# Kernel tuning notes

Measured on AMD Instinct MI355X. Metric: run time of the kernel, lower is better.

Reference implementation:

```python
import jax, jax.numpy as jnp
import numpy as np

B, N, D, H, E = 4, 1024, 1024, 2048, 8

def setup_inputs() -> dict:
    key = jax.random.key(0)
    ks = jax.random.split(key, 5)
    return {
        "x": jax.random.normal(ks[0], (B, N, D), dtype=jnp.float32),
        "gate_w": jax.random.normal(ks[1], (D, E), dtype=jnp.float32) * 0.02,
        "gate_b": jnp.zeros((E,), dtype=jnp.float32),
        "w1": jax.random.normal(ks[2], (E, D, H), dtype=jnp.float32) * 0.02,
        "b1": jnp.zeros((E, H), dtype=jnp.float32),
        "w2": jax.random.normal(ks[3], (E, H, D), dtype=jnp.float32) * 0.02,
        "b2": jnp.zeros((E, D), dtype=jnp.float32),
        "gamma": jnp.ones((D,), dtype=jnp.float32),
    }

def reference(x, gate_w, gate_b, w1, b1, w2, b2, gamma):
    b, n, d = x.shape
    e = w1.shape[0]
    xf = x.reshape(b * n, d)                                    # [T, D]
    # gate: softmax over experts, then top-1
    probs = jax.nn.softmax(xf @ gate_w + gate_b, axis=-1)       # [T, E]
    top_val = jnp.max(probs, axis=-1, keepdims=True)            # [T, 1]
    top_idx = jnp.argmax(probs, axis=-1)                        # [T]
    # all-expert FFN (dense reference for masked dispatch; dropout in eval)
    h = jax.nn.gelu(jnp.einsum('td,edh->eth', xf, w1) + b1[:, None, :],
                    approximate=False)                          # [E, T, H]
    eo = jnp.einsum('eth,ehd->etd', h, w2) + b2[:, None, :]     # [E, T, D]
    onehot = jax.nn.one_hot(top_idx, e, dtype=xf.dtype)         # [T, E]
    out = jnp.einsum('etd,te->td', eo, onehot)                  # select routed expert
    y = (xf + out * top_val).reshape(b, n, d)
    # RMSNorm: F.normalize (L2, eps=1e-12) * gamma * sqrt(dim)
    nrm = jnp.linalg.norm(y, axis=-1, keepdims=True)
    y = y / jnp.maximum(nrm, 1e-12) * gamma * np.float32(np.sqrt(d))
    # load-balancing loss (unbiased variance like torch.var)
    importance = probs.sum(axis=0)                              # [E]
    load_loss = jnp.var(importance, ddof=1) / (jnp.mean(importance) ** 2 + 1e-10)
    return jax.nn.gelu(y, approximate=False), load_loss
```

## Files before the change

kernel.cpp:

```cpp
#include <hip/hip_runtime.h>
#include <math.h>

#define T_TOK 4096
#define DIM   1024
#define HID   2048
#define NE    8
#define TMM   128
#define BK    64
#define GATE_BLOCKS (T_TOK / 4)

typedef unsigned int  u32;
typedef unsigned short u16;
typedef __attribute__((ext_vector_type(8))) short bf16x8;
typedef __attribute__((ext_vector_type(4))) float f32x4;

__device__ __forceinline__ float gelu_exact(float v) {
    return 0.5f * v * (1.0f + erff(v * 0.70710678118654752440f));
}

__device__ __forceinline__ float gelu_fast(float x) {
    float u = 1.5957691216057308f * (x + 0.044715f * x * x * x);
    float e = __expf(u);
    float t = 1.f - 2.f / (e + 1.f);
    return 0.5f * x * (1.f + t);
}

__device__ __forceinline__ u16 f2bf(float v) {
    u32 u = __float_as_uint(v);
    u32 r = (u + 0x7FFFu + ((u >> 16) & 1u)) >> 16;
    return (u16)r;
}

__device__ __forceinline__ void gld_lds16(const void* g, void* l) {
    __builtin_amdgcn_global_load_lds(
        (const __attribute__((address_space(1))) u32*)g,
        (__attribute__((address_space(3))) u32*)l,
        16, 0, 0);
}

__device__ __forceinline__ void transpose_body(
    const float* __restrict__ in, u16* __restrict__ out, int R, int C,
    int bx, int by, int bz, float (*tile)[65])
{
    const float* src = in  + (size_t)bz * R * C;
    u16*         dst = out + (size_t)bz * R * C;
    const int c0 = bx * 64, r0 = by * 64;
    const int th = threadIdx.x;

    const int tr  = th >> 4;
    const int tc4 = (th & 15) * 4;
    #pragma unroll
    for (int i = 0; i < 4; i++) {
        const int r = tr + i * 16;
        float4 v = *(const float4*)&src[(size_t)(r0 + r) * C + c0 + tc4];
        tile[r][tc4 + 0] = v.x; tile[r][tc4 + 1] = v.y;
        tile[r][tc4 + 2] = v.z; tile[r][tc4 + 3] = v.w;
    }
    __syncthreads();
    const int cc  = th >> 4;
    const int rr4 = (th & 15) * 4;
    #pragma unroll
    for (int i = 0; i < 4; i++) {
        const int c = cc + i * 16;
        ushort4 o;
        o.x = f2bf(tile[rr4 + 0][c]);
        o.y = f2bf(tile[rr4 + 1][c]);
        o.z = f2bf(tile[rr4 + 2][c]);
        o.w = f2bf(tile[rr4 + 3][c]);
        *(ushort4*)&dst[(size_t)(c0 + c) * R + r0 + rr4] = o;
    }
}

__global__ __launch_bounds__(256) void prep_kernel(
    const float* __restrict__ w1, const float* __restrict__ w2,
    u16* __restrict__ w1t, u16* __restrict__ w2t,
    const float* __restrict__ x, const float* __restrict__ gw,
    const float* __restrict__ gb, float* __restrict__ top_val,
    int* __restrict__ top_idx, float* __restrict__ partial_imp,
    int* __restrict__ partial_cnt)
{
    __shared__ float tile[64][65];
    __shared__ float s_imp[NE];
    __shared__ int   s_cnt[NE];

    const int id = blockIdx.x;
    if (id < 4096) {
        transpose_body(w1, w1t, DIM, HID, id & 31, (id >> 5) & 15, id >> 9, tile);
        return;
    }
    if (id < 8192) {
        const int i2 = id - 4096;
        transpose_body(w2, w2t, HID, DIM, i2 & 15, (i2 >> 4) & 31, i2 >> 9, tile);
        return;
    }

    const int g = id - 8192;
    if (threadIdx.x < NE) { s_imp[threadIdx.x] = 0.f; s_cnt[threadIdx.x] = 0; }
    __syncthreads();

    const int wave = threadIdx.x >> 6;
    const int lane = threadIdx.x & 63;
    const int t = g * 4 + wave;

    float acc[NE];
    #pragma unroll
    for (int e = 0; e < NE; e++) acc[e] = 0.f;

    const float* xr = x + (size_t)t * DIM;
    #pragma unroll 4
    for (int k = lane; k < DIM; k += 64) {
        float xv = xr[k];
        const float* gp = gw + (size_t)k * NE;
        float4 g0 = *(const float4*)gp;
        float4 g1 = *(const float4*)(gp + 4);
        acc[0] += xv * g0.x; acc[1] += xv * g0.y;
        acc[2] += xv * g0.z; acc[3] += xv * g0.w;
        acc[4] += xv * g1.x; acc[5] += xv * g1.y;
        acc[6] += xv * g1.z; acc[7] += xv * g1.w;
    }
    #pragma unroll
    for (int e = 0; e < NE; e++) {
        #pragma unroll
        for (int off = 32; off > 0; off >>= 1)
            acc[e] += __shfl_down(acc[e], off, 64);
    }
    if (lane == 0) {
        float l[NE];
        float m = -1e30f;
        #pragma unroll
        for (int e = 0; e < NE; e++) { l[e] = acc[e] + gb[e]; m = fmaxf(m, l[e]); }
        float s = 0.f;
        #pragma unroll
        for (int e = 0; e < NE; e++) { l[e] = expf(l[e] - m); s += l[e]; }
        float inv = 1.f / s;
        int bi = 0; float bv = -1.f;
        #pragma unroll
        for (int e = 0; e < NE; e++) {
            float p = l[e] * inv;
            atomicAdd(&s_imp[e], p);
            if (p > bv) { bv = p; bi = e; }
        }
        top_val[t] = bv;
        top_idx[t] = bi;
        atomicAdd(&s_cnt[bi], 1);
    }
    __syncthreads();
    if (threadIdx.x < NE) {
        partial_imp[g * NE + threadIdx.x] = s_imp[threadIdx.x];
        partial_cnt[g * NE + threadIdx.x] = s_cnt[threadIdx.x];
    }
}

__global__ __launch_bounds__(256) void plan_kernel(
    const float* __restrict__ partial_imp, const int* __restrict__ partial_cnt,
    int* __restrict__ counts, int* __restrict__ offsets,
    int* __restrict__ tile_e, int* __restrict__ tile_s,
    int* __restrict__ tile_rows, int* __restrict__ ntiles,
    float* __restrict__ loss_out)
{
    __shared__ float rimp[32][NE];
    __shared__ int   rcnt[32][NE];
    const int th = threadIdx.x;
    const int e = th & 7, chunk = th >> 3;
    float si = 0.f; int sc = 0;
    #pragma unroll 8
    for (int i = 0; i < GATE_BLOCKS / 32; i++) {
        const int b = chunk * (GATE_BLOCKS / 32) + i;
        si += partial_imp[b * NE + e];
        sc += partial_cnt[b * NE + e];
    }
    rimp[chunk][e] = si;
    rcnt[chunk][e] = sc;
    __syncthreads();
    if (th < NE) {
        float s = 0.f; int c = 0;
        for (int i = 0; i < 32; i++) { s += rimp[i][th]; c += rcnt[i][th]; }
        counts[th] = c;
        rimp[0][th] = s;
        rcnt[0][th] = c;
    }
    __syncthreads();
    if (th == 0) {
        int off = 0, nt = 0;
        for (int ee = 0; ee < NE; ee++) {
            offsets[ee] = off;
            const int c = rcnt[0][ee];
            for (int s = 0; s < c; s += TMM) {
                tile_e[nt] = ee;
                tile_s[nt] = off + s;
                tile_rows[nt] = min(TMM, c - s);
                nt++;
            }
            off += c;
        }
        offsets[NE] = off;
        *ntiles = nt;

        float mean = 0.f;
        for (int ee = 0; ee < NE; ee++) mean += rimp[0][ee];
        mean *= (1.0f / NE);
        float var = 0.f;
        for (int ee = 0; ee < NE; ee++) { float d = rimp[0][ee] - mean; var += d * d; }
        var *= (1.0f / (NE - 1));
        loss_out[0] = var / (mean * mean + 1e-10f);
    }
}

__global__ __launch_bounds__(256) void scatter_kernel(
    const int* __restrict__ top_idx, const int* __restrict__ offsets,
    int* __restrict__ cursors, int* __restrict__ sorted_tok)
{
    __shared__ int lcnt[NE], lbase[NE];
    if (threadIdx.x < NE) lcnt[threadIdx.x] = 0;
    __syncthreads();
    const int t = blockIdx.x * blockDim.x + threadIdx.x;
    const int e = top_idx[t];
    const int lrank = atomicAdd(&lcnt[e], 1);
    __syncthreads();
    if (threadIdx.x < NE)
        lbase[threadIdx.x] = atomicAdd(&cursors[threadIdx.x], lcnt[threadIdx.x]);
    __syncthreads();
    sorted_tok[offsets[e] + lbase[e] + lrank] = t;
}

__global__ __launch_bounds__(256) void gather_x_kernel(
    const float* __restrict__ x, const int* __restrict__ sorted_tok,
    u16* __restrict__ xs)
{
    const int s = blockIdx.x;
    const int tok = sorted_tok[s];
    const float* src = x + (size_t)tok * DIM;
    u16* dst = xs + (size_t)s * DIM;
    const int i = threadIdx.x * 4;
    float4 v = *(const float4*)&src[i];
    ushort4 o;
    o.x = f2bf(v.x); o.y = f2bf(v.y); o.z = f2bf(v.z); o.w = f2bf(v.w);
    *(ushort4*)&dst[i] = o;
}

__global__ __launch_bounds__(512, 4) void ffn1_mfma(
    const u16* __restrict__ xs, const u16* __restrict__ w1t,
    const float* __restrict__ b1,
    const int* __restrict__ tile_e, const int* __restrict__ tile_s,
    const int* __restrict__ tile_rows, const int* __restrict__ ntiles,
    u16* __restrict__ h_buf)
{
    const int tile = blockIdx.y;
    if (tile >= *ntiles) return;
    const int e     = tile_e[tile];
    const int sbase = tile_s[tile];
    const int rows  = tile_rows[tile];
    const int nbase = blockIdx.x * 256;

    __shared__ __align__(16) u16 As[128 * BK];
    __shared__ __align__(16) u16 Bs[256 * BK];

    const int th = threadIdx.x;
    const int w  = th >> 6;
    const int l  = th & 63;
    const int wm = w >> 2, wn = w & 3;
    const int lr = l >> 3;
    const int lcs = ((l & 7) ^ lr) * 8;

    const u16* aptr[2];
    #pragma unroll
    for (int c = 0; c < 2; c++) {
        int srow = sbase + c * 64 + w * 8 + lr;
        if (srow > T_TOK - 1) srow = T_TOK - 1;
        aptr[c] = xs + (size_t)srow * DIM + lcs;
    }
    const u16* wb = w1t + (size_t)e * HID * DIM + (size_t)nbase * DIM;
    const u16* bptr[4];
    #pragma unroll
    for (int c = 0; c < 4; c++)
        bptr[c] = wb + (size_t)(c * 64 + w * 8 + lr) * DIM + lcs;

    f32x4 acc[4][4] = {};

    for (int k0 = 0; k0 < DIM; k0 += BK) {
        __syncthreads();
        #pragma unroll
        for (int c = 0; c < 2; c++)
            gld_lds16(aptr[c] + k0, &As[(c * 64 + w * 8) * BK]);
        #pragma unroll
        for (int c = 0; c < 4; c++)
            gld_lds16(bptr[c] + k0, &Bs[(c * 64 + w * 8) * BK]);
        __syncthreads();
        #pragma unroll
        for (int ks = 0; ks < 2; ks++) {
            const int ko = ((ks * 4 + (l >> 4)) ^ (l & 7)) * 8;
            bf16x8 af[4], bfr[4];
            #pragma unroll
            for (int i = 0; i < 4; i++)
                af[i]  = *(const bf16x8*)&As[(wm * 64 + i * 16 + (l & 15)) * BK + ko];
            #pragma unroll
            for (int i = 0; i < 4; i++)
                bfr[i] = *(const bf16x8*)&Bs[(wn * 64 + i * 16 + (l & 15)) * BK + ko];
            #pragma unroll
            for (int mi = 0; mi < 4; mi++)
                #pragma unroll
                for (int ni = 0; ni < 4; ni++)
                    acc[mi][ni] = __builtin_amdgcn_mfma_f32_16x16x32_bf16(
                        af[mi], bfr[ni], acc[mi][ni], 0, 0, 0);
        }
    }

    const int col = l & 15, quad = l >> 4;
    #pragma unroll
    for (int ni = 0; ni < 4; ni++) {
        const int n = nbase + wn * 64 + ni * 16 + col;
        const float bias = b1[e * HID + n];
        #pragma unroll
        for (int mi = 0; mi < 4; mi++) {
            #pragma unroll
            for (int r = 0; r < 4; r++) {
                const int m = wm * 64 + mi * 16 + quad * 4 + r;
                if (m < rows) {
                    float v = acc[mi][ni][r] + bias;
                    h_buf[(size_t)(sbase + m) * HID + n] = f2bf(gelu_fast(v));
                }
            }
        }
    }
}

__global__ __launch_bounds__(256) void ffn2_mfma(
    const u16* __restrict__ h_buf, const u16* __restrict__ w2t,
    const float* __restrict__ b2, const float* __restrict__ x,
    const int* __restrict__ sorted_tok, const float* __restrict__ top_val,
    const int* __restrict__ tile_e, const int* __restrict__ tile_s,
    const int* __restrict__ tile_rows, const int* __restrict__ ntiles,
    float* __restrict__ yout)
{
    const int tile = blockIdx.y;
    if (tile >= *ntiles) return;
    const int e     = tile_e[tile];
    const int sbase = tile_s[tile];
    const int rows  = tile_rows[tile];
    const int nbase = blockIdx.x * 128;

    __shared__ __align__(16) u16 As[128 * BK];
    __shared__ __align__(16) u16 Bs[128 * BK];

    const int th = threadIdx.x;
    const int w  = th >> 6;
    const int l  = th & 63;
    const int wm = w >> 1, wn = w & 1;
    const int lr = l >> 3;
    const int lcs = ((l & 7) ^ lr) * 8;

    const u16* aptr[4];
    #pragma unroll
    for (int c = 0; c < 4; c++) {
        int srow = sbase + w * 32 + c * 8 + lr;
        if (srow > T_TOK - 1) srow = T_TOK - 1;
        aptr[c] = h_buf + (size_t)srow * HID + lcs;
    }
    const u16* wb = w2t + (size_t)e * DIM * HID + (size_t)nbase * HID;
    const u16* bptr[4];
    #pragma unroll
    for (int c = 0; c < 4; c++)
        bptr[c] = wb + (size_t)(w * 32 + c * 8 + lr) * HID + lcs;

    f32x4 acc[4][4] = {};

    for (int k0 = 0; k0 < HID; k0 += BK) {
        __syncthreads();
        #pragma unroll
        for (int c = 0; c < 4; c++)
            gld_lds16(aptr[c] + k0, &As[(w * 32 + c * 8) * BK]);
        #pragma unroll
        for (int c = 0; c < 4; c++)
            gld_lds16(bptr[c] + k0, &Bs[(w * 32 + c * 8) * BK]);
        __syncthreads();
        #pragma unroll
        for (int ks = 0; ks < 2; ks++) {
            const int ko = ((ks * 4 + (l >> 4)) ^ (l & 7)) * 8;
            bf16x8 af[4], bfr[4];
            #pragma unroll
            for (int i = 0; i < 4; i++)
                af[i]  = *(const bf16x8*)&As[(wm * 64 + i * 16 + (l & 15)) * BK + ko];
            #pragma unroll
            for (int i = 0; i < 4; i++)
                bfr[i] = *(const bf16x8*)&Bs[(wn * 64 + i * 16 + (l & 15)) * BK + ko];
            #pragma unroll
            for (int mi = 0; mi < 4; mi++)
                #pragma unroll
                for (int ni = 0; ni < 4; ni++)
                    acc[mi][ni] = __builtin_amdgcn_mfma_f32_16x16x32_bf16(
                        af[mi], bfr[ni], acc[mi][ni], 0, 0, 0);
        }
    }

    const int col = l & 15, quad = l >> 4;
    float bias[4];
    #pragma unroll
    for (int ni = 0; ni < 4; ni++)
        bias[ni] = b2[e * DIM + nbase + wn * 64 + ni * 16 + col];

    #pragma unroll
    for (int mi = 0; mi < 4; mi++) {
        #pragma unroll
        for (int r = 0; r < 4; r++) {
            const int m = wm * 64 + mi * 16 + quad * 4 + r;
            if (m < rows) {
                const int t = sorted_tok[sbase + m];
                const float tv = top_val[t];
                #pragma unroll
                for (int ni = 0; ni < 4; ni++) {
                    const int n = nbase + wn * 64 + ni * 16 + col;
                    float v = acc[mi][ni][r] + bias[ni];
                    yout[(size_t)t * DIM + n] = x[(size_t)t * DIM + n] + v * tv;
                }
            }
        }
    }
}

__global__ __launch_bounds__(256) void norm_kernel(float* __restrict__ y,
                                                   const float* __restrict__ gamma)
{
    const int t = blockIdx.x;
    float* row = y + (size_t)t * DIM;
    const int th = threadIdx.x;
    float4 v = *(const float4*)&row[th * 4];
    float ss = v.x * v.x + v.y * v.y + v.z * v.z + v.w * v.w;

    const int lane = th & 63, wave = th >> 6;
    #pragma unroll
    for (int off = 32; off > 0; off >>= 1) ss += __shfl_down(ss, off, 64);
    __shared__ float red[4];
    if (lane == 0) red[wave] = ss;
    __syncthreads();
    float total = red[0] + red[1] + red[2] + red[3];

    float nrm = sqrtf(total);
    float scale = 32.0f / fmaxf(nrm, 1e-12f);

    float4 g = *(const float4*)&gamma[th * 4];
    float4 o;
    o.x = gelu_exact(v.x * scale * g.x);
    o.y = gelu_exact(v.y * scale * g.y);
    o.z = gelu_exact(v.z * scale * g.z);
    o.w = gelu_exact(v.w * scale * g.w);
    *(float4*)&row[th * 4] = o;
}

extern "C" void kernel_launch(void* const* d_in, const int* in_sizes, int n_in,
                              void* d_out, int out_size, void* d_ws, size_t ws_size,
                              hipStream_t stream) {
    const float* x      = (const float*)d_in[0];
    const float* gate_w = (const float*)d_in[1];
    const float* gate_b = (const float*)d_in[2];
    const float* w1     = (const float*)d_in[3];
    const float* b1     = (const float*)d_in[4];
    const float* w2     = (const float*)d_in[5];
    const float* b2     = (const float*)d_in[6];
    const float* gamma  = (const float*)d_in[7];

    float* out  = (float*)d_out;
    float* loss = out + (size_t)T_TOK * DIM;

    char* ws = (char*)d_ws;
    float* top_val     = (float*)(ws + 0);
    int*   top_idx     = (int*)  (ws + 16384);
    int*   sorted_tok  = (int*)  (ws + 32768);
    int*   counts      = (int*)  (ws + 49152);
    int*   cursors     = (int*)  (ws + 49216);
    int*   offsets     = (int*)  (ws + 49280);
    int*   tile_e      = (int*)  (ws + 49664);
    int*   tile_s      = (int*)  (ws + 50176);
    int*   tile_rows   = (int*)  (ws + 50688);
    int*   ntiles      = (int*)  (ws + 51200);
    float* partial_imp = (float*)(ws + 65536);
    int*   partial_cnt = (int*)  (ws + 98304);
    u16*   x_sorted    = (u16*)  (ws + 131072);
    u16*   h_buf       = (u16*)  (ws + 131072 + 8388608);
    u16*   w1t         = (u16*)  (ws + 131072 + 8388608 + 16777216);
    u16*   w2t         = (u16*)  (ws + 131072 + 8388608 + 16777216 + 33554432);

    hipMemsetAsync(ws + 49216, 0, 64, stream);

    prep_kernel<<<8192 + GATE_BLOCKS, 256, 0, stream>>>(
        w1, w2, w1t, w2t, x, gate_w, gate_b, top_val, top_idx,
        partial_imp, partial_cnt);
    plan_kernel<<<1, 256, 0, stream>>>(partial_imp, partial_cnt, counts,
                                       offsets, tile_e, tile_s, tile_rows,
                                       ntiles, loss);
    scatter_kernel<<<T_TOK / 256, 256, 0, stream>>>(top_idx, offsets, cursors,
                                                    sorted_tok);
    gather_x_kernel<<<T_TOK, 256, 0, stream>>>(x, sorted_tok, x_sorted);

    ffn1_mfma<<<dim3(HID / 256, 40), 512, 0, stream>>>(
        x_sorted, w1t, b1, tile_e, tile_s, tile_rows, ntiles, h_buf);
    ffn2_mfma<<<dim3(DIM / 128, 40), 256, 0, stream>>>(
        h_buf, w2t, b2, x, sorted_tok, top_val, tile_e, tile_s, tile_rows,
        ntiles, out);
    norm_kernel<<<T_TOK, 256, 0, stream>>>(out, gamma);
}
```

Baseline: 300.3 us.

## Retile expert GEMMs: smaller ffn1 N-tile, 64-row ffn2 tiles, wider transpose stores

ffn1 goes from 512-thread 128x256 tiles to 256-thread 128x128 tiles, which doubles the block count along the hidden dimension. ffn2 uses a second tile plan with 64-row M tiles, which doubles the tiles per expert so more blocks cover the fixed 1024 output columns and fewer MFMA rows are wasted on each expert's last tile. The weight transpose now writes 8 bf16 values per store instead of 4. The aim is better CU occupancy and load balance for the grouped GEMMs, at the cost of less reuse of B per block and more weight traffic in ffn2.

```diff
diff --git a/kernel.cpp b/kernel.cpp
--- a/kernel.cpp
+++ b/kernel.cpp
@@ -6,12 +6,14 @@
 #define HID   2048
 #define NE    8
 #define TMM   128
+#define TM2   64
 #define BK    64
 #define GATE_BLOCKS (T_TOK / 4)
 
 typedef unsigned int  u32;
 typedef unsigned short u16;
 typedef __attribute__((ext_vector_type(8))) short bf16x8;
+typedef __attribute__((ext_vector_type(8))) unsigned short u16x8;
 typedef __attribute__((ext_vector_type(4))) float f32x4;
 
 __device__ __forceinline__ float gelu_exact(float v) {
@@ -57,17 +59,15 @@
         tile[r][tc4 + 2] = v.z; tile[r][tc4 + 3] = v.w;
     }
     __syncthreads();
-    const int cc  = th >> 4;
-    const int rr4 = (th & 15) * 4;
-    #pragma unroll
-    for (int i = 0; i < 4; i++) {
-        const int c = cc + i * 16;
-        ushort4 o;
-        o.x = f2bf(tile[rr4 + 0][c]);
-        o.y = f2bf(tile[rr4 + 1][c]);
-        o.z = f2bf(tile[rr4 + 2][c]);
-        o.w = f2bf(tile[rr4 + 3][c]);
-        *(ushort4*)&dst[(size_t)(c0 + c) * R + r0 + rr4] = o;
+    const int cc  = th >> 3;
+    const int rr8 = (th & 7) * 8;
+    #pragma unroll
+    for (int i = 0; i < 2; i++) {
+        const int c = cc + i * 32;
+        u16x8 o;
+        #pragma unroll
+        for (int j = 0; j < 8; j++) o[j] = f2bf(tile[rr8 + j][c]);
+        *(u16x8*)&dst[(size_t)(c0 + c) * R + r0 + rr8] = o;
     }
 }
 
@@ -156,6 +156,8 @@
     int* __restrict__ counts, int* __restrict__ offsets,
     int* __restrict__ tile_e, int* __restrict__ tile_s,
     int* __restrict__ tile_rows, int* __restrict__ ntiles,
+    int* __restrict__ tile2_e, int* __restrict__ tile2_s,
+    int* __restrict__ tile2_rows, int* __restrict__ ntiles2,
     float* __restrict__ loss_out)
 {
     __shared__ float rimp[32][NE];
@@ -181,7 +183,7 @@
     }
     __syncthreads();
     if (th == 0) {
-        int off = 0, nt = 0;
+        int off = 0, nt = 0, nt2 = 0;
         for (int ee = 0; ee < NE; ee++) {
             offsets[ee] = off;
             const int c = rcnt[0][ee];
@@ -191,10 +193,17 @@
                 tile_rows[nt] = min(TMM, c - s);
                 nt++;
             }
+            for (int s = 0; s < c; s += TM2) {
+                tile2_e[nt2] = ee;
+                tile2_s[nt2] = off + s;
+                tile2_rows[nt2] = min(TM2, c - s);
+                nt2++;
+            }
             off += c;
         }
         offsets[NE] = off;
-        *ntiles = nt;
+        *ntiles  = nt;
+        *ntiles2 = nt2;
 
         float mean = 0.f;
         for (int ee = 0; ee < NE; ee++) mean += rimp[0][ee];
@@ -238,7 +247,7 @@
     *(ushort4*)&dst[i] = o;
 }
 
-__global__ __launch_bounds__(512, 4) void ffn1_mfma(
+__global__ __launch_bounds__(256) void ffn1_mfma(
     const u16* __restrict__ xs, const u16* __restrict__ w1t,
     const float* __restrict__ b1,
     const int* __restrict__ tile_e, const int* __restrict__ tile_s,
@@ -250,22 +259,22 @@
     const int e     = tile_e[tile];
     const int sbase = tile_s[tile];
     const int rows  = tile_rows[tile];
-    const int nbase = blockIdx.x * 256;
+    const int nbase = blockIdx.x * 128;
 
     __shared__ __align__(16) u16 As[128 * BK];
-    __shared__ __align__(16) u16 Bs[256 * BK];
+    __shared__ __align__(16) u16 Bs[128 * BK];
 
     const int th = threadIdx.x;
     const int w  = th >> 6;
     const int l  = th & 63;
-    const int wm = w >> 2, wn = w & 3;
+    const int wm = w >> 1, wn = w & 1;
     const int lr = l >> 3;
     const int lcs = ((l & 7) ^ lr) * 8;
 
-    const u16* aptr[2];
-    #pragma unroll
-    for (int c = 0; c < 2; c++) {
-        int srow = sbase + c * 64 + w * 8 + lr;
+    const u16* aptr[4];
+    #pragma unroll
+    for (int c = 0; c < 4; c++) {
+        int srow = sbase + w * 32 + c * 8 + lr;
         if (srow > T_TOK - 1) srow = T_TOK - 1;
         aptr[c] = xs + (size_t)srow * DIM + lcs;
     }
@@ -273,18 +282,18 @@
     const u16* bptr[4];
     #pragma unroll
     for (int c = 0; c < 4; c++)
-        bptr[c] = wb + (size_t)(c * 64 + w * 8 + lr) * DIM + lcs;
+        bptr[c] = wb + (size_t)(w * 32 + c * 8 + lr) * DIM + lcs;
 
     f32x4 acc[4][4] = {};
 
     for (int k0 = 0; k0 < DIM; k0 += BK) {
         __syncthreads();
         #pragma unroll
-        for (int c = 0; c < 2; c++)
-            gld_lds16(aptr[c] + k0, &As[(c * 64 + w * 8) * BK]);
-        #pragma unroll
         for (int c = 0; c < 4; c++)
-            gld_lds16(bptr[c] + k0, &Bs[(c * 64 + w * 8) * BK]);
+            gld_lds16(aptr[c] + k0, &As[(w * 32 + c * 8) * BK]);
+        #pragma unroll
+        for (int c = 0; c < 4; c++)
+            gld_lds16(bptr[c] + k0, &Bs[(w * 32 + c * 8) * BK]);
         __syncthreads();
         #pragma unroll
         for (int ks = 0; ks < 2; ks++) {
@@ -328,18 +337,18 @@
     const u16* __restrict__ h_buf, const u16* __restrict__ w2t,
     const float* __restrict__ b2, const float* __restrict__ x,
     const int* __restrict__ sorted_tok, const float* __restrict__ top_val,
-    const int* __restrict__ tile_e, const int* __restrict__ tile_s,
-    const int* __restrict__ tile_rows, const int* __restrict__ ntiles,
+    const int* __restrict__ tile2_e, const int* __restrict__ tile2_s,
+    const int* __restrict__ tile2_rows, const int* __restrict__ ntiles2,
     float* __restrict__ yout)
 {
     const int tile = blockIdx.y;
-    if (tile >= *ntiles) return;
-    const int e     = tile_e[tile];
-    const int sbase = tile_s[tile];
-    const int rows  = tile_rows[tile];
+    if (tile >= *ntiles2) return;
+    const int e     = tile2_e[tile];
+    const int sbase = tile2_s[tile];
+    const int rows  = tile2_rows[tile];
     const int nbase = blockIdx.x * 128;
 
-    __shared__ __align__(16) u16 As[128 * BK];
+    __shared__ __align__(16) u16 As[64 * BK];
     __shared__ __align__(16) u16 Bs[128 * BK];
 
     const int th = threadIdx.x;
@@ -349,10 +358,10 @@
     const int lr = l >> 3;
     const int lcs = ((l & 7) ^ lr) * 8;
 
-    const u16* aptr[4];
-    #pragma unroll
-    for (int c = 0; c < 4; c++) {
-        int srow = sbase + w * 32 + c * 8 + lr;
+    const u16* aptr[2];
+    #pragma unroll
+    for (int c = 0; c < 2; c++) {
+        int srow = sbase + c * 32 + w * 8 + lr;
         if (srow > T_TOK - 1) srow = T_TOK - 1;
         aptr[c] = h_buf + (size_t)srow * HID + lcs;
     }
@@ -360,31 +369,31 @@
     const u16* bptr[4];
     #pragma unroll
     for (int c = 0; c < 4; c++)
-        bptr[c] = wb + (size_t)(w * 32 + c * 8 + lr) * HID + lcs;
-
-    f32x4 acc[4][4] = {};
+        bptr[c] = wb + (size_t)(c * 32 + w * 8 + lr) * HID + lcs;
+
+    f32x4 acc[2][4] = {};
 
     for (int k0 = 0; k0 < HID; k0 += BK) {
         __syncthreads();
         #pragma unroll
+        for (int c = 0; c < 2; c++)
+            gld_lds16(aptr[c] + k0, &As[(c * 32 + w * 8) * BK]);
+        #pragma unroll
         for (int c = 0; c < 4; c++)
-            gld_lds16(aptr[c] + k0, &As[(w * 32 + c * 8) * BK]);
-        #pragma unroll
-        for (int c = 0; c < 4; c++)
-            gld_lds16(bptr[c] + k0, &Bs[(w * 32 + c * 8) * BK]);
+            gld_lds16(bptr[c] + k0, &Bs[(c * 32 + w * 8) * BK]);
         __syncthreads();
         #pragma unroll
         for (int ks = 0; ks < 2; ks++) {
             const int ko = ((ks * 4 + (l >> 4)) ^ (l & 7)) * 8;
-            bf16x8 af[4], bfr[4];
-            #pragma unroll
-            for (int i = 0; i < 4; i++)
-                af[i]  = *(const bf16x8*)&As[(wm * 64 + i * 16 + (l & 15)) * BK + ko];
+            bf16x8 af[2], bfr[4];
+            #pragma unroll
+            for (int i = 0; i < 2; i++)
+                af[i]  = *(const bf16x8*)&As[(wm * 32 + i * 16 + (l & 15)) * BK + ko];
             #pragma unroll
             for (int i = 0; i < 4; i++)
                 bfr[i] = *(const bf16x8*)&Bs[(wn * 64 + i * 16 + (l & 15)) * BK + ko];
             #pragma unroll
-            for (int mi = 0; mi < 4; mi++)
+            for (int mi = 0; mi < 2; mi++)
                 #pragma unroll
                 for (int ni = 0; ni < 4; ni++)
                     acc[mi][ni] = __builtin_amdgcn_mfma_f32_16x16x32_bf16(
@@ -399,10 +408,10 @@
         bias[ni] = b2[e * DIM + nbase + wn * 64 + ni * 16 + col];
 
     #pragma unroll
-    for (int mi = 0; mi < 4; mi++) {
+    for (int mi = 0; mi < 2; mi++) {
         #pragma unroll
         for (int r = 0; r < 4; r++) {
-            const int m = wm * 64 + mi * 16 + quad * 4 + r;
+            const int m = wm * 32 + mi * 16 + quad * 4 + r;
             if (m < rows) {
                 const int t = sorted_tok[sbase + m];
                 const float tv = top_val[t];
@@ -472,6 +481,10 @@
     int*   tile_s      = (int*)  (ws + 50176);
     int*   tile_rows   = (int*)  (ws + 50688);
     int*   ntiles      = (int*)  (ws + 51200);
+    int*   tile2_e     = (int*)  (ws + 51712);
+    int*   tile2_s     = (int*)  (ws + 52736);
+    int*   tile2_rows  = (int*)  (ws + 53760);
+    int*   ntiles2     = (int*)  (ws + 54784);
     float* partial_imp = (float*)(ws + 65536);
     int*   partial_cnt = (int*)  (ws + 98304);
     u16*   x_sorted    = (u16*)  (ws + 131072);
@@ -486,15 +499,16 @@
         partial_imp, partial_cnt);
     plan_kernel<<<1, 256, 0, stream>>>(partial_imp, partial_cnt, counts,
                                        offsets, tile_e, tile_s, tile_rows,
-                                       ntiles, loss);
+                                       ntiles, tile2_e, tile2_s, tile2_rows,
+                                       ntiles2, loss);
     scatter_kernel<<<T_TOK / 256, 256, 0, stream>>>(top_idx, offsets, cursors,
                                                     sorted_tok);
     gather_x_kernel<<<T_TOK, 256, 0, stream>>>(x, sorted_tok, x_sorted);
 
-    ffn1_mfma<<<dim3(HID / 256, 40), 512, 0, stream>>>(
+    ffn1_mfma<<<dim3(HID / 128, 40), 256, 0, stream>>>(
         x_sorted, w1t, b1, tile_e, tile_s, tile_rows, ntiles, h_buf);
-    ffn2_mfma<<<dim3(DIM / 128, 40), 256, 0, stream>>>(
-        h_buf, w2t, b2, x, sorted_tok, top_val, tile_e, tile_s, tile_rows,
-        ntiles, out);
+    ffn2_mfma<<<dim3(DIM / 128, 80), 256, 0, stream>>>(
+        h_buf, w2t, b2, x, sorted_tok, top_val, tile2_e, tile2_s, tile2_rows,
+        ntiles2, out);
     norm_kernel<<<T_TOK, 256, 0, stream>>>(out, gamma);
 }
```

Measured after the change: 310.1 us. 1.03x slower.
